# Optimization experiments

Measured on AMD Instinct MI355X. Metric: run time of the kernel, lower is better.

The kernel has to match this reference:

```python
import jax, jax.numpy as jnp
import numpy as np

N, L, H, D, NCLS = 8192, 1024, 512, 256, 2


def setup_inputs() -> dict:
    key = jax.random.key(0)
    ks = jax.random.split(key, 11)
    s = 0.02  # xavier-ish init scale
    return {
        "x": jax.random.normal(ks[0], (N, L), jnp.float32),
        "W_fc": jax.random.normal(ks[1], (L, H), jnp.float32) * s,
        "b_fc": jnp.zeros((H,), jnp.float32),
        "W_a": jax.random.normal(ks[2], (H, D), jnp.float32) * s,
        "b_a": jnp.zeros((D,), jnp.float32),
        "W_b": jax.random.normal(ks[3], (H, D), jnp.float32) * s,
        "b_b": jnp.zeros((D,), jnp.float32),
        "W_c": jax.random.normal(ks[4], (D, 1), jnp.float32) * s,
        "b_c": jnp.zeros((1,), jnp.float32),
        "W_cls": jax.random.normal(ks[5], (H, NCLS), jnp.float32) * s,
        "b_cls": jnp.zeros((NCLS,), jnp.float32),
    }


def reference(x, W_fc, b_fc, W_a, b_a, W_b, b_b, W_c, b_c, W_cls, b_cls):
    n = x.shape[0]
    # fc: Linear + ReLU (dropout p=0, eval)
    h = jax.nn.relu(x @ W_fc + b_fc)                      # [N, 512]
    # gated attention net (Attn_Net_Gated, n_classes=1)
    a = jnp.tanh(h @ W_a + b_a)                           # [N, 256]
    b = jax.nn.sigmoid(h @ W_b + b_b)                     # [N, 256]
    scores = ((a * b) @ W_c + b_c)[:, 0]                  # [N] diagonal scores
    # A_raw: the original's wasteful CxNxN diagonal matrix (C=1)
    idx = jnp.arange(n)
    A_raw = jnp.zeros((1, n, n), x.dtype).at[0, idx, idx].set(scores)
    # bag_forward: softmax over all N*N entries (N^2 - N zeros off-diagonal),
    # then M = (A @ h).sum(dim=1). Closed form, numerically stable:
    m = jnp.maximum(jnp.max(scores), jnp.zeros((), x.dtype))
    e = jnp.exp(scores - m)                               # diag exp terms
    e0 = jnp.exp(-m)                                      # off-diag exp(0 - m)
    Z = jnp.sum(e) + (n * n - n) * e0
    s = e / Z                                             # softmaxed diagonal
    # row_i @ h = s_i*h_i + (1/Z)*sum_{j!=i} h_j ; sum over i:
    M = s @ h + ((n - 1) * e0 / Z) * jnp.sum(h, axis=0)   # [512]
    logits = M @ W_cls + b_cls                            # [2]
    return (logits[None, :], A_raw)
```

## Files before the change

kernel.cpp:

```cpp
#include <hip/hip_runtime.h>
#include <stdint.h>

#define NROWS 8192
#define LDIM  1024
#define HDIM  512

typedef __attribute__((ext_vector_type(8))) short short8;
typedef __attribute__((ext_vector_type(4))) float f32x4;
typedef __attribute__((ext_vector_type(4))) unsigned int u32x4;

typedef __attribute__((address_space(3))) unsigned int lds_uint;
typedef const __attribute__((address_space(1))) unsigned int glob_uint;

#define ZN_TOTAL 16777215L
#define Z_MEGA_START 0L
#define Z_MEGA_CNT   6291455L
#define ZB_MEGA      3072
#define Z_G1_START   6291455L
#define Z_G1_CNT     5242880L
#define ZB_G1        2560
#define Z_G2_START   11534335L
#define Z_G2_CNT     3670016L
#define ZB_G2        1792
#define Z_SC_START   15204351L
#define Z_SC_PER     768L

__device__ __forceinline__ void llds16(const void* g, void* l) {
  __builtin_amdgcn_global_load_lds((glob_uint*)g, (lds_uint*)l, 16, 0, 0);
}

__device__ __forceinline__ unsigned short f2bf(float f) {
  union { float f; unsigned int u; } c; c.f = f;
  unsigned int u = c.u;
  unsigned int r = (u + 0x7fffu + ((u >> 16) & 1u)) >> 16;
  return (unsigned short)r;
}

__device__ __forceinline__ float bfbits2f(unsigned int hi16) {
  union { unsigned int u; float f; } c; c.u = hi16;
  return c.f;
}

__device__ __forceinline__ void zero_chunks(u32x4* __restrict__ out16, long c0, long c1, int tid) {
  u32x4 z = {0u, 0u, 0u, 0u};
  for (long i = c0 + tid; i < c1; i += 256) out16[i] = z;
}

__global__ __launch_bounds__(256) void mega_bw_kernel(const float* __restrict__ x,
                                                      const float* __restrict__ Wfc,
                                                      const float* __restrict__ Wa,
                                                      const float* __restrict__ Wb,
                                                      unsigned short* __restrict__ xb,
                                                      unsigned short* __restrict__ WfcT,
                                                      unsigned short* __restrict__ WabT,
                                                      float* __restrict__ out) {
  __shared__ float tile[32][33];
  const int bid = blockIdx.x;
  const int tid = threadIdx.x;
  if (bid < ZB_MEGA) {
    long c0 = Z_MEGA_START + (long)bid * 2048;
    long c1 = c0 + 2048 < Z_MEGA_START + Z_MEGA_CNT ? c0 + 2048 : Z_MEGA_START + Z_MEGA_CNT;
    zero_chunks((u32x4*)(out + 4), c0, c1, tid);
    if (bid == 0 && tid == 0) {
      out[2] = 0.f; out[3] = 0.f;
      out[67108864] = 0.f; out[67108865] = 0.f;
    }
    return;
  }
  if (bid < ZB_MEGA + 4096) {
    long i = ((long)(bid - ZB_MEGA) * 256 + tid) * 8;
    float4 v0 = *(const float4*)(x + i);
    float4 v1 = *(const float4*)(x + i + 4);
    union { unsigned short s[8]; uint4 u; } o;
    o.s[0] = f2bf(v0.x); o.s[1] = f2bf(v0.y); o.s[2] = f2bf(v0.z); o.s[3] = f2bf(v0.w);
    o.s[4] = f2bf(v1.x); o.s[5] = f2bf(v1.y); o.s[6] = f2bf(v1.z); o.s[7] = f2bf(v1.w);
    *(uint4*)(xb + i) = o.u;
    return;
  }
  int tt = bid - (ZB_MEGA + 4096);
  const float* src; unsigned short* dst; int srcn, dstk, k0, n0;
  if (tt < 512) {
    src = Wfc; dst = WfcT; srcn = 512; dstk = 1024;
    k0 = (tt >> 4) * 32; n0 = (tt & 15) * 32;
  } else if (tt < 640) {
    int t2 = tt - 512;
    src = Wa; dst = WabT; srcn = 256; dstk = 512;
    k0 = (t2 >> 3) * 32; n0 = (t2 & 7) * 32;
  } else {
    int t2 = tt - 640;
    src = Wb; dst = WabT + 256 * 512; srcn = 256; dstk = 512;
    k0 = (t2 >> 3) * 32; n0 = (t2 & 7) * 32;
  }
  int r = tid >> 3, c4 = (tid & 7) * 4;
  float4 v = *(const float4*)(src + (long)(k0 + r) * srcn + n0 + c4);
  tile[r][c4 + 0] = v.x; tile[r][c4 + 1] = v.y; tile[r][c4 + 2] = v.z; tile[r][c4 + 3] = v.w;
  __syncthreads();
  union { unsigned short s[4]; uint2 u; } o;
#pragma unroll
  for (int j = 0; j < 4; ++j) o.s[j] = f2bf(tile[c4 + j][r]);
  *(uint2*)(dst + (long)(n0 + r) * dstk + k0 + c4) = o.u;
}

template <int EPI>
__global__ __launch_bounds__(256) void gemm_bt(const unsigned short* __restrict__ A,
                                               const unsigned short* __restrict__ Bt,
                                               const float* __restrict__ bias,
                                               void* __restrict__ out,
                                               int M, int N, int K,
                                               float* __restrict__ zout, long zstart, long zcount) {
  constexpr int BM = 128, BN = 128, BK = 32;
  __shared__ unsigned short sA[2][BM * BK];
  __shared__ unsigned short sB[2][BN * BK];
  const int tid = threadIdx.x;
  const int nbn = N / BN;
  const int ncomp = (M / BM) * nbn;
  if ((int)blockIdx.x >= ncomp) {
    int zb = (int)blockIdx.x - ncomp;
    long c0 = zstart + (long)zb * 2048;
    long lim = zstart + zcount;
    long c1 = c0 + 2048 < lim ? c0 + 2048 : lim;
    zero_chunks((u32x4*)(zout + 4), c0, c1, tid);
    return;
  }
  const int lane = tid & 63;
  const int wv = tid >> 6;
  const int wm = wv >> 1;
  const int wn = wv & 1;
  const int bm = blockIdx.x / nbn, bn = blockIdx.x % nbn;
  const int row0 = bm * BM, col0 = bn * BN;

  f32x4 acc[4][4] = {};
  const int nk = K / BK;

  auto stage = [&](int buf, int kt) {
#pragma unroll
    for (int r = 0; r < 2; ++r) {
      int c = r * 256 + tid;
      int arow = c >> 2, acb = (c & 3) * 8;
      const unsigned short* g = A + (long)(row0 + arow) * K + kt * BK + acb;
      unsigned short* l = (unsigned short*)&sA[buf][(r * 256 + wv * 64) * 8];
      llds16(g, l);
    }
#pragma unroll
    for (int r = 0; r < 2; ++r) {
      int c = r * 256 + tid;
      int brow = c >> 2, bcb = (c & 3) * 8;
      const unsigned short* g = Bt + (long)(col0 + brow) * K + kt * BK + bcb;
      unsigned short* l = (unsigned short*)&sB[buf][(r * 256 + wv * 64) * 8];
      llds16(g, l);
    }
  };

  stage(0, 0);
  __syncthreads();

  for (int kt = 0; kt < nk; ++kt) {
    int cur = kt & 1;
    if (kt + 1 < nk) stage(cur ^ 1, kt + 1);
    const unsigned short* bA = sA[cur];
    const unsigned short* bB = sB[cur];
    short8 af[4], bfr[4];
#pragma unroll
    for (int fm = 0; fm < 4; ++fm)
      af[fm] = *(const short8*)&bA[(wm * 64 + fm * 16 + (lane & 15)) * BK + (lane >> 4) * 8];
#pragma unroll
    for (int fn = 0; fn < 4; ++fn)
      bfr[fn] = *(const short8*)&bB[(wn * 64 + fn * 16 + (lane & 15)) * BK + (lane >> 4) * 8];
#pragma unroll
    for (int fm = 0; fm < 4; ++fm)
#pragma unroll
      for (int fn = 0; fn < 4; ++fn)
        acc[fm][fn] = __builtin_amdgcn_mfma_f32_16x16x32_bf16(af[fm], bfr[fn], acc[fm][fn], 0, 0, 0);
    __syncthreads();
  }

#pragma unroll
  for (int fm = 0; fm < 4; ++fm) {
#pragma unroll
    for (int fn = 0; fn < 4; ++fn) {
#pragma unroll
      for (int i = 0; i < 4; ++i) {
        int row = row0 + wm * 64 + fm * 16 + (lane >> 4) * 4 + i;
        int col = col0 + wn * 64 + fn * 16 + (lane & 15);
        float v = acc[fm][fn][i];
        if (EPI == 0) {
          v += bias[col];
          v = v > 0.f ? v : 0.f;
          ((unsigned short*)out)[(long)row * N + col] = f2bf(v);
        } else {
          ((float*)out)[(long)row * N + col] = v;
        }
      }
    }
  }
}

__global__ __launch_bounds__(256) void score_kernel(const float* __restrict__ t,
                                                    const float* __restrict__ ba,
                                                    const float* __restrict__ bb,
                                                    const float* __restrict__ Wc,
                                                    const float* __restrict__ bc,
                                                    float* __restrict__ scores,
                                                    float* __restrict__ out ) {
  {
    long c0 = Z_SC_START + (long)blockIdx.x * Z_SC_PER;
    zero_chunks((u32x4*)(out + 4), c0, c0 + Z_SC_PER, threadIdx.x);
  }
  int row = blockIdx.x * 4 + (threadIdx.x >> 6);
  int lane = threadIdx.x & 63;
  const float* tr = t + (long)row * 512;
  float s = 0.f;
#pragma unroll
  for (int j = 0; j < 4; ++j) {
    int d = lane + j * 64;
    float u = tr[d] + ba[d];
    float v = tr[d + 256] + bb[d];
    float av = tanhf(u);
    float bv = 1.f / (1.f + __expf(-v));
    s += av * bv * Wc[d];
  }
#pragma unroll
  for (int off = 32; off; off >>= 1) s += __shfl_down(s, off);
  if (lane == 0) scores[row] = s + bc[0];
}

__global__ __launch_bounds__(1024) void reduce_kernel(const float* __restrict__ scores,
                                                      float* __restrict__ w,
                                                      float* __restrict__ out) {
  __shared__ float red[1024];
  int t = threadIdx.x;
  float v[8];
  float mx = -1e30f;
#pragma unroll
  for (int j = 0; j < 8; ++j) { v[j] = scores[t * 8 + j]; mx = fmaxf(mx, v[j]); }
#pragma unroll
  for (int j = 0; j < 8; ++j) out[2 + 8193L * (t * 8 + j)] = v[j];
  red[t] = mx; __syncthreads();
  for (int s = 512; s; s >>= 1) { if (t < s) red[t] = fmaxf(red[t], red[t + s]); __syncthreads(); }
  float m = fmaxf(red[0], 0.f);
  __syncthreads();
  float e[8]; float se = 0.f;
#pragma unroll
  for (int j = 0; j < 8; ++j) { e[j] = __expf(v[j] - m); se += e[j]; }
  red[t] = se; __syncthreads();
  for (int s = 512; s; s >>= 1) { if (t < s) red[t] += red[t + s]; __syncthreads(); }
  float e0 = __expf(-m);
  float Z = red[0] + 67100672.0f * e0;
  float c0 = 8191.0f * e0 / Z;
#pragma unroll
  for (int j = 0; j < 8; ++j) w[t * 8 + j] = e[j] / Z + c0;
}

__global__ __launch_bounds__(256) void wsum_kernel(const unsigned short* __restrict__ h,
                                                   const float* __restrict__ w,
                                                   float* __restrict__ part) {
  int b = blockIdx.x;
  int t = threadIdx.x;
  float a0 = 0.f, a1 = 0.f;
  for (int i = b * 128; i < b * 128 + 128; ++i) {
    float wi = w[i];
    unsigned int hv = *(const unsigned int*)&h[(long)i * 512 + t * 2];
    a0 += wi * bfbits2f(hv << 16);
    a1 += wi * bfbits2f(hv & 0xffff0000u);
  }
  part[b * 512 + t * 2] = a0;
  part[b * 512 + t * 2 + 1] = a1;
}

__global__ __launch_bounds__(512) void final_kernel(const float* __restrict__ part,
                                                    const float* __restrict__ Wcls,
                                                    const float* __restrict__ bcls,
                                                    float* __restrict__ out) {
  __shared__ float Msh[512];
  int t = threadIdx.x;
  float s = 0.f;
  for (int b = 0; b < 64; ++b) s += part[b * 512 + t];
  Msh[t] = s;
  __syncthreads();
  if (t < 64) {
    float p0 = 0.f, p1 = 0.f;
    for (int j = t; j < 512; j += 64) { p0 += Msh[j] * Wcls[j * 2]; p1 += Msh[j] * Wcls[j * 2 + 1]; }
#pragma unroll
    for (int off = 32; off; off >>= 1) { p0 += __shfl_down(p0, off); p1 += __shfl_down(p1, off); }
    if (t == 0) { out[0] = p0 + bcls[0]; out[1] = p1 + bcls[1]; }
  }
}

extern "C" void kernel_launch(void* const* d_in, const int* in_sizes, int n_in,
                              void* d_out, int out_size, void* d_ws, size_t ws_size,
                              hipStream_t stream) {
  const float* x    = (const float*)d_in[0];
  const float* Wfc  = (const float*)d_in[1];
  const float* bfc  = (const float*)d_in[2];
  const float* Wa   = (const float*)d_in[3];
  const float* ba   = (const float*)d_in[4];
  const float* Wb   = (const float*)d_in[5];
  const float* bb   = (const float*)d_in[6];
  const float* Wc   = (const float*)d_in[7];
  const float* bc   = (const float*)d_in[8];
  const float* Wcls = (const float*)d_in[9];
  const float* bcls = (const float*)d_in[10];
  float* out = (float*)d_out;
  char* ws = (char*)d_ws;

  unsigned short* xb     = (unsigned short*)(ws + 0);
  unsigned short* WfcT   = (unsigned short*)(ws + 16777216);
  unsigned short* WabT   = (unsigned short*)(ws + 17825792);
  unsigned short* hbuf   = (unsigned short*)(ws + 18350080);
  float*          tbuf   = (float*)(ws + 26738688);
  float*          scores = (float*)(ws + 43515904);
  float*          wbuf   = (float*)(ws + 43548672);
  float*          part   = (float*)(ws + 43581440);

  mega_bw_kernel<<<ZB_MEGA + 4096 + 768, 256, 0, stream>>>(x, Wfc, Wa, Wb, xb, WfcT, WabT, out);
  gemm_bt<0><<<(NROWS / 128) * (HDIM / 128) + ZB_G1, 256, 0, stream>>>(
      xb, WfcT, bfc, hbuf, NROWS, HDIM, LDIM, out, Z_G1_START, Z_G1_CNT);
  gemm_bt<1><<<(NROWS / 128) * (HDIM / 128) + ZB_G2, 256, 0, stream>>>(
      hbuf, WabT, nullptr, tbuf, NROWS, HDIM, HDIM, out, Z_G2_START, Z_G2_CNT);
  score_kernel<<<NROWS / 4, 256, 0, stream>>>(tbuf, ba, bb, Wc, bc, scores, out);
  reduce_kernel<<<1, 1024, 0, stream>>>(scores, wbuf, out);
  wsum_kernel<<<64, 256, 0, stream>>>(hbuf, wbuf, part);
  final_kernel<<<1, 512, 0, stream>>>(part, Wcls, bcls, out);
}
```

Before: 117.4 us.

## Fuse gated-attention scoring into second GEMM epilogue and merge softmax reduction with weighted sum

Interleaves the Wa and Wb columns in the transposed weight layout so that each warp's GEMM2 tile holds matching tanh and sigmoid inputs. The gate, the Wc dot product and a per-row partial score are then computed in the epilogue, which removes the fp32 t buffer round trip and the separate score kernel. The softmax max and sum reduction is merged into the weighted-sum kernel: each of its 64 blocks recomputes the global reduction redundantly, replacing two launches with one. The diagonal score writes move to extra blocks of the final kernel, and the zero-fill ranges are rebalanced across kernels. The trade-off is redundant reduction work in every block and heavier GEMM2 epilogue math.

```diff
diff --git a/kernel.cpp b/kernel.cpp
--- a/kernel.cpp
+++ b/kernel.cpp
@@ -12,18 +12,18 @@
 typedef __attribute__((address_space(3))) unsigned int lds_uint;
 typedef const __attribute__((address_space(1))) unsigned int glob_uint;
 
-#define ZN_TOTAL 16777215L
 #define Z_MEGA_START 0L
-#define Z_MEGA_CNT   6291455L
-#define ZB_MEGA      3072
-#define Z_G1_START   6291455L
+#define Z_MEGA_CNT   6815744L
+#define ZB_MEGA      3328
+#define Z_G1_START   6815744L
 #define Z_G1_CNT     5242880L
 #define ZB_G1        2560
-#define Z_G2_START   11534335L
-#define Z_G2_CNT     3670016L
-#define ZB_G2        1792
-#define Z_SC_START   15204351L
-#define Z_SC_PER     768L
+#define Z_G2_START   12058624L
+#define Z_G2_CNT     4194304L
+#define ZB_G2        2048
+#define Z_RW_START   16252928L
+#define Z_RW_CNT     524287L
+#define ZB_RW        256
 
 __device__ __forceinline__ void llds16(const void* g, void* l) {
   __builtin_amdgcn_global_load_lds((glob_uint*)g, (lds_uint*)l, 16, 0, 0);
@@ -59,7 +59,8 @@
   const int tid = threadIdx.x;
   if (bid < ZB_MEGA) {
     long c0 = Z_MEGA_START + (long)bid * 2048;
-    long c1 = c0 + 2048 < Z_MEGA_START + Z_MEGA_CNT ? c0 + 2048 : Z_MEGA_START + Z_MEGA_CNT;
+    long lim = Z_MEGA_START + Z_MEGA_CNT;
+    long c1 = c0 + 2048 < lim ? c0 + 2048 : lim;
     zero_chunks((u32x4*)(out + 4), c0, c1, tid);
     if (bid == 0 && tid == 0) {
       out[2] = 0.f; out[3] = 0.f;
@@ -78,17 +79,17 @@
     return;
   }
   int tt = bid - (ZB_MEGA + 4096);
-  const float* src; unsigned short* dst; int srcn, dstk, k0, n0;
+  const float* src; unsigned short* dst; int srcn, dstk, k0, n0; int mode;
   if (tt < 512) {
-    src = Wfc; dst = WfcT; srcn = 512; dstk = 1024;
+    src = Wfc; dst = WfcT; srcn = 512; dstk = 1024; mode = 0;
     k0 = (tt >> 4) * 32; n0 = (tt & 15) * 32;
   } else if (tt < 640) {
     int t2 = tt - 512;
-    src = Wa; dst = WabT; srcn = 256; dstk = 512;
+    src = Wa; dst = WabT; srcn = 256; dstk = 512; mode = 1;
     k0 = (t2 >> 3) * 32; n0 = (t2 & 7) * 32;
   } else {
     int t2 = tt - 640;
-    src = Wb; dst = WabT + 256 * 512; srcn = 256; dstk = 512;
+    src = Wb; dst = WabT; srcn = 256; dstk = 512; mode = 2;
     k0 = (t2 >> 3) * 32; n0 = (t2 & 7) * 32;
   }
   int r = tid >> 3, c4 = (tid & 7) * 4;
@@ -98,16 +99,19 @@
   union { unsigned short s[4]; uint2 u; } o;
 #pragma unroll
   for (int j = 0; j < 4; ++j) o.s[j] = f2bf(tile[c4 + j][r]);
-  *(uint2*)(dst + (long)(n0 + r) * dstk + k0 + c4) = o.u;
-}
-
-template <int EPI>
-__global__ __launch_bounds__(256) void gemm_bt(const unsigned short* __restrict__ A,
-                                               const unsigned short* __restrict__ Bt,
-                                               const float* __restrict__ bias,
-                                               void* __restrict__ out,
-                                               int M, int N, int K,
-                                               float* __restrict__ zout, long zstart, long zcount) {
+  int n = n0 + r;
+  long crow;
+  if (mode == 0) crow = n;
+  else crow = (long)(((n >> 4) << 5) + (n & 15) + (mode == 2 ? 16 : 0));
+  *(uint2*)(dst + crow * dstk + k0 + c4) = o.u;
+}
+
+__global__ __launch_bounds__(256) void gemm1_kernel(const unsigned short* __restrict__ A,
+                                                    const unsigned short* __restrict__ Bt,
+                                                    const float* __restrict__ bias,
+                                                    unsigned short* __restrict__ out,
+                                                    int M, int N, int K,
+                                                    float* __restrict__ zout) {
   constexpr int BM = 128, BN = 128, BK = 32;
   __shared__ unsigned short sA[2][BM * BK];
   __shared__ unsigned short sB[2][BN * BK];
@@ -116,8 +120,8 @@
   const int ncomp = (M / BM) * nbn;
   if ((int)blockIdx.x >= ncomp) {
     int zb = (int)blockIdx.x - ncomp;
-    long c0 = zstart + (long)zb * 2048;
-    long lim = zstart + zcount;
+    long c0 = Z_G1_START + (long)zb * 2048;
+    long lim = Z_G1_START + Z_G1_CNT;
     long c1 = c0 + 2048 < lim ? c0 + 2048 : lim;
     zero_chunks((u32x4*)(zout + 4), c0, c1, tid);
     return;
@@ -182,84 +186,156 @@
       for (int i = 0; i < 4; ++i) {
         int row = row0 + wm * 64 + fm * 16 + (lane >> 4) * 4 + i;
         int col = col0 + wn * 64 + fn * 16 + (lane & 15);
-        float v = acc[fm][fn][i];
-        if (EPI == 0) {
-          v += bias[col];
-          v = v > 0.f ? v : 0.f;
-          ((unsigned short*)out)[(long)row * N + col] = f2bf(v);
-        } else {
-          ((float*)out)[(long)row * N + col] = v;
-        }
+        float v = acc[fm][fn][i] + bias[col];
+        v = v > 0.f ? v : 0.f;
+        out[(long)row * N + col] = f2bf(v);
       }
     }
   }
 }
 
-__global__ __launch_bounds__(256) void score_kernel(const float* __restrict__ t,
-                                                    const float* __restrict__ ba,
-                                                    const float* __restrict__ bb,
-                                                    const float* __restrict__ Wc,
-                                                    const float* __restrict__ bc,
-                                                    float* __restrict__ scores,
-                                                    float* __restrict__ out ) {
-  {
-    long c0 = Z_SC_START + (long)blockIdx.x * Z_SC_PER;
-    zero_chunks((u32x4*)(out + 4), c0, c0 + Z_SC_PER, threadIdx.x);
-  }
-  int row = blockIdx.x * 4 + (threadIdx.x >> 6);
-  int lane = threadIdx.x & 63;
-  const float* tr = t + (long)row * 512;
-  float s = 0.f;
-#pragma unroll
-  for (int j = 0; j < 4; ++j) {
-    int d = lane + j * 64;
-    float u = tr[d] + ba[d];
-    float v = tr[d + 256] + bb[d];
-    float av = tanhf(u);
-    float bv = 1.f / (1.f + __expf(-v));
-    s += av * bv * Wc[d];
-  }
-#pragma unroll
-  for (int off = 32; off; off >>= 1) s += __shfl_down(s, off);
-  if (lane == 0) scores[row] = s + bc[0];
-}
-
-__global__ __launch_bounds__(1024) void reduce_kernel(const float* __restrict__ scores,
-                                                      float* __restrict__ w,
+__global__ __launch_bounds__(256) void gemm2_fused(const unsigned short* __restrict__ A,
+                                                   const unsigned short* __restrict__ Bt,
+                                                   const float* __restrict__ ba_,
+                                                   const float* __restrict__ bb_,
+                                                   const float* __restrict__ Wc,
+                                                   float* __restrict__ spart,
+                                                   float* __restrict__ zout) {
+  constexpr int BM = 128, BN = 128, BK = 32;
+  constexpr int M = NROWS, N = HDIM, K = HDIM;
+  __shared__ unsigned short sA[2][BM * BK];
+  __shared__ unsigned short sB[2][BN * BK];
+  const int tid = threadIdx.x;
+  const int nbn = N / BN;
+  const int ncomp = (M / BM) * nbn;
+  if ((int)blockIdx.x >= ncomp) {
+    int zb = (int)blockIdx.x - ncomp;
+    long c0 = Z_G2_START + (long)zb * 2048;
+    long lim = Z_G2_START + Z_G2_CNT;
+    long c1 = c0 + 2048 < lim ? c0 + 2048 : lim;
+    zero_chunks((u32x4*)(zout + 4), c0, c1, tid);
+    return;
+  }
+  const int lane = tid & 63;
+  const int wv = tid >> 6;
+  const int wm = wv >> 1;
+  const int wn = wv & 1;
+  const int bm = blockIdx.x / nbn, bn = blockIdx.x % nbn;
+  const int row0 = bm * BM, col0 = bn * BN;
+
+  f32x4 acc[4][4] = {};
+  const int nk = K / BK;
+
+  auto stage = [&](int buf, int kt) {
+#pragma unroll
+    for (int r = 0; r < 2; ++r) {
+      int c = r * 256 + tid;
+      int arow = c >> 2, acb = (c & 3) * 8;
+      const unsigned short* g = A + (long)(row0 + arow) * K + kt * BK + acb;
+      unsigned short* l = (unsigned short*)&sA[buf][(r * 256 + wv * 64) * 8];
+      llds16(g, l);
+    }
+#pragma unroll
+    for (int r = 0; r < 2; ++r) {
+      int c = r * 256 + tid;
+      int brow = c >> 2, bcb = (c & 3) * 8;
+      const unsigned short* g = Bt + (long)(col0 + brow) * K + kt * BK + bcb;
+      unsigned short* l = (unsigned short*)&sB[buf][(r * 256 + wv * 64) * 8];
+      llds16(g, l);
+    }
+  };
+
+  stage(0, 0);
+  __syncthreads();
+
+  for (int kt = 0; kt < nk; ++kt) {
+    int cur = kt & 1;
+    if (kt + 1 < nk) stage(cur ^ 1, kt + 1);
+    const unsigned short* bA = sA[cur];
+    const unsigned short* bB = sB[cur];
+    short8 af[4], bfr[4];
+#pragma unroll
+    for (int fm = 0; fm < 4; ++fm)
+      af[fm] = *(const short8*)&bA[(wm * 64 + fm * 16 + (lane & 15)) * BK + (lane >> 4) * 8];
+#pragma unroll
+    for (int fn = 0; fn < 4; ++fn)
+      bfr[fn] = *(const short8*)&bB[(wn * 64 + fn * 16 + (lane & 15)) * BK + (lane >> 4) * 8];
+#pragma unroll
+    for (int fm = 0; fm < 4; ++fm)
+#pragma unroll
+      for (int fn = 0; fn < 4; ++fn)
+        acc[fm][fn] = __builtin_amdgcn_mfma_f32_16x16x32_bf16(af[fm], bfr[fn], acc[fm][fn], 0, 0, 0);
+    __syncthreads();
+  }
+
+  const int colbase = col0 + wn * 64;
+  const int d0 = (colbase >> 5) * 16 + (lane & 15);
+  float wc0 = Wc[d0],  wc1 = Wc[d0 + 16];
+  float av0 = ba_[d0], av1 = ba_[d0 + 16];
+  float bv0 = bb_[d0], bv1 = bb_[d0 + 16];
+  float* sp = spart + (long)(bn * 2 + wn) * NROWS;
+#pragma unroll
+  for (int fm = 0; fm < 4; ++fm) {
+#pragma unroll
+    for (int i = 0; i < 4; ++i) {
+      float a0 = acc[fm][0][i] + av0, b0 = acc[fm][1][i] + bv0;
+      float a1 = acc[fm][2][i] + av1, b1 = acc[fm][3][i] + bv1;
+      float v = tanhf(a0) * (1.f / (1.f + __expf(-b0))) * wc0
+              + tanhf(a1) * (1.f / (1.f + __expf(-b1))) * wc1;
+#pragma unroll
+      for (int off = 1; off < 16; off <<= 1) v += __shfl_xor(v, off);
+      if ((lane & 15) == 0) {
+        int row = row0 + wm * 64 + fm * 16 + (lane >> 4) * 4 + i;
+        sp[row] = v;
+      }
+    }
+  }
+}
+
+__global__ __launch_bounds__(256) void redwsum_kernel(const float* __restrict__ spart,
+                                                      const float* __restrict__ bc,
+                                                      const unsigned short* __restrict__ h,
+                                                      float* __restrict__ part,
                                                       float* __restrict__ out) {
-  __shared__ float red[1024];
-  int t = threadIdx.x;
-  float v[8];
-  float mx = -1e30f;
-#pragma unroll
-  for (int j = 0; j < 8; ++j) { v[j] = scores[t * 8 + j]; mx = fmaxf(mx, v[j]); }
-#pragma unroll
-  for (int j = 0; j < 8; ++j) out[2 + 8193L * (t * 8 + j)] = v[j];
-  red[t] = mx; __syncthreads();
-  for (int s = 512; s; s >>= 1) { if (t < s) red[t] = fmaxf(red[t], red[t + s]); __syncthreads(); }
+  const int b = blockIdx.x;
+  const int t = threadIdx.x;
+  if (b >= 64) {
+    int zb = b - 64;
+    long c0 = Z_RW_START + (long)zb * 2048;
+    long lim = Z_RW_START + Z_RW_CNT;
+    long c1 = c0 + 2048 < lim ? c0 + 2048 : lim;
+    zero_chunks((u32x4*)(out + 4), c0, c1, t);
+    return;
+  }
+  __shared__ float sc[NROWS];
+  __shared__ float red[256];
+  __shared__ float warr[128];
+  const float bcv = bc[0];
+  float lmax = -1e30f;
+  for (int k = t; k < NROWS; k += 256) {
+    float s = bcv;
+#pragma unroll
+    for (int q = 0; q < 8; ++q) s += spart[q * NROWS + k];
+    sc[k] = s;
+    lmax = fmaxf(lmax, s);
+  }
+  red[t] = lmax; __syncthreads();
+  for (int s = 128; s; s >>= 1) { if (t < s) red[t] = fmaxf(red[t], red[t + s]); __syncthreads(); }
   float m = fmaxf(red[0], 0.f);
   __syncthreads();
-  float e[8]; float se = 0.f;
-#pragma unroll
-  for (int j = 0; j < 8; ++j) { e[j] = __expf(v[j] - m); se += e[j]; }
-  red[t] = se; __syncthreads();
-  for (int s = 512; s; s >>= 1) { if (t < s) red[t] += red[t + s]; __syncthreads(); }
+  float lsum = 0.f;
+  for (int k = t; k < NROWS; k += 256) lsum += __expf(sc[k] - m);
+  red[t] = lsum; __syncthreads();
+  for (int s = 128; s; s >>= 1) { if (t < s) red[t] += red[t + s]; __syncthreads(); }
   float e0 = __expf(-m);
   float Z = red[0] + 67100672.0f * e0;
-  float c0 = 8191.0f * e0 / Z;
-#pragma unroll
-  for (int j = 0; j < 8; ++j) w[t * 8 + j] = e[j] / Z + c0;
-}
-
-__global__ __launch_bounds__(256) void wsum_kernel(const unsigned short* __restrict__ h,
-                                                   const float* __restrict__ w,
-                                                   float* __restrict__ part) {
-  int b = blockIdx.x;
-  int t = threadIdx.x;
+  float c0w = 8191.0f * e0 / Z;
+  if (t < 128) warr[t] = __expf(sc[b * 128 + t] - m) / Z + c0w;
+  __syncthreads();
   float a0 = 0.f, a1 = 0.f;
-  for (int i = b * 128; i < b * 128 + 128; ++i) {
-    float wi = w[i];
-    unsigned int hv = *(const unsigned int*)&h[(long)i * 512 + t * 2];
+  for (int i = 0; i < 128; ++i) {
+    float wi = warr[i];
+    unsigned int hv = *(const unsigned int*)&h[(long)(b * 128 + i) * 512 + t * 2];
     a0 += wi * bfbits2f(hv << 16);
     a1 += wi * bfbits2f(hv & 0xffff0000u);
   }
@@ -268,11 +344,23 @@
 }
 
 __global__ __launch_bounds__(512) void final_kernel(const float* __restrict__ part,
+                                                    const float* __restrict__ spart,
+                                                    const float* __restrict__ bc,
                                                     const float* __restrict__ Wcls,
                                                     const float* __restrict__ bcls,
                                                     float* __restrict__ out) {
+  const int t = threadIdx.x;
+  if (blockIdx.x > 0) {
+    if (t < 256) {
+      int row = (blockIdx.x - 1) * 256 + t;
+      float s = bc[0];
+#pragma unroll
+      for (int q = 0; q < 8; ++q) s += spart[q * NROWS + row];
+      out[2 + 8193L * row] = s;
+    }
+    return;
+  }
   __shared__ float Msh[512];
-  int t = threadIdx.x;
   float s = 0.f;
   for (int b = 0; b < 64; ++b) s += part[b * 512 + t];
   Msh[t] = s;
@@ -303,22 +391,18 @@
   float* out = (float*)d_out;
   char* ws = (char*)d_ws;
 
-  unsigned short* xb     = (unsigned short*)(ws + 0);
-  unsigned short* WfcT   = (unsigned short*)(ws + 16777216);
-  unsigned short* WabT   = (unsigned short*)(ws + 17825792);
-  unsigned short* hbuf   = (unsigned short*)(ws + 18350080);
-  float*          tbuf   = (float*)(ws + 26738688);
-  float*          scores = (float*)(ws + 43515904);
-  float*          wbuf   = (float*)(ws + 43548672);
-  float*          part   = (float*)(ws + 43581440);
+  unsigned short* xb    = (unsigned short*)(ws + 0);
+  unsigned short* WfcT  = (unsigned short*)(ws + 16777216);
+  unsigned short* WabT  = (unsigned short*)(ws + 17825792);
+  unsigned short* hbuf  = (unsigned short*)(ws + 18350080);
+  float*          spart = (float*)(ws + 26738688);
+  float*          part  = (float*)(ws + 27000832);
 
   mega_bw_kernel<<<ZB_MEGA + 4096 + 768, 256, 0, stream>>>(x, Wfc, Wa, Wb, xb, WfcT, WabT, out);
-  gemm_bt<0><<<(NROWS / 128) * (HDIM / 128) + ZB_G1, 256, 0, stream>>>(
-      xb, WfcT, bfc, hbuf, NROWS, HDIM, LDIM, out, Z_G1_START, Z_G1_CNT);
-  gemm_bt<1><<<(NROWS / 128) * (HDIM / 128) + ZB_G2, 256, 0, stream>>>(
-      hbuf, WabT, nullptr, tbuf, NROWS, HDIM, HDIM, out, Z_G2_START, Z_G2_CNT);
-  score_kernel<<<NROWS / 4, 256, 0, stream>>>(tbuf, ba, bb, Wc, bc, scores, out);
-  reduce_kernel<<<1, 1024, 0, stream>>>(scores, wbuf, out);
-  wsum_kernel<<<64, 256, 0, stream>>>(hbuf, wbuf, part);
-  final_kernel<<<1, 512, 0, stream>>>(part, Wcls, bcls, out);
-}
+  gemm1_kernel<<<(NROWS / 128) * (HDIM / 128) + ZB_G1, 256, 0, stream>>>(
+      xb, WfcT, bfc, hbuf, NROWS, HDIM, LDIM, out);
+  gemm2_fused<<<(NROWS / 128) * (HDIM / 128) + ZB_G2, 256, 0, stream>>>(
+      hbuf, WabT, ba, bb, Wc, spart, out);
+  redwsum_kernel<<<64 + ZB_RW, 256, 0, stream>>>(spart, bc, hbuf, part, out);
+  final_kernel<<<33, 512, 0, stream>>>(part, spart, bc, Wcls, bcls, out);
+}
```

Measured after the change: 118.3 us. No clear change (+0.7%).
